# Performance work log

Hardware: AMD Instinct MI355X
Metric: run time of the kernel (lower is better)

## Reference

```python
import jax, jax.numpy as jnp
import numpy as np

NUM_HEADS = 8
NEG_MASK = -1000.0  # original code masks with -1000, not -inf


def setup_inputs() -> dict:
    key = jax.random.key(0)
    ks = jax.random.split(key, 12)
    B, S, D = 4, 2048, 512
    HID, OUT = 512, 512
    dh = D // NUM_HEADS      # 64, per-head input dim
    eh = HID // NUM_HEADS    # 64, per-head hidden dim
    w = 0.02
    return {
        "q": jax.random.normal(ks[0], (B, S, D), dtype=jnp.float32),
        "k": jax.random.normal(ks[1], (B, S, D), dtype=jnp.float32),
        "v": jax.random.normal(ks[2], (B, S, D), dtype=jnp.float32),
        # Linear weights stored as [in, out] (transpose of torch convention)
        "Wq": jax.random.normal(ks[3], (dh, eh), dtype=jnp.float32) * w,
        "bq": jax.random.normal(ks[4], (eh,), dtype=jnp.float32) * w,
        "Wk": jax.random.normal(ks[5], (dh, eh), dtype=jnp.float32) * w,
        "bk": jax.random.normal(ks[6], (eh,), dtype=jnp.float32) * w,
        "Wv": jax.random.normal(ks[7], (dh, eh), dtype=jnp.float32) * w,
        "bv": jax.random.normal(ks[8], (eh,), dtype=jnp.float32) * w,
        "Wo": jax.random.normal(ks[9], (HID, OUT), dtype=jnp.float32) * w,
        "bo": jax.random.normal(ks[10], (OUT,), dtype=jnp.float32) * w,
        "valid_lens": jnp.maximum(jax.random.randint(ks[11], (B,), 0, S), 1),
        "max_len": S,
    }


def reference(q, k, v, Wq, bq, Wk, bk, Wv, bv, Wo, bo, valid_lens, max_len):
    B, S, D = q.shape
    H = NUM_HEADS
    # split into heads: [B, S, H, dh]; note the SAME projection weights are
    # shared across heads (as in the original module)
    qh = q.reshape(B, S, H, D // H)
    kh = k.reshape(B, S, H, D // H)
    vh = v.reshape(B, S, H, D // H)
    qp = jnp.einsum('bshd,de->bshe', qh, Wq) + bq  # [B,S,H,eh]
    kp = jnp.einsum('bshd,de->bshe', kh, Wk) + bk
    vp = jnp.einsum('bshd,de->bshe', vh, Wv) + bv
    scale = 1.0 / jnp.sqrt(jnp.asarray(qp.shape[-1], qp.dtype))
    scores = jnp.einsum('bshe,bthe->bhst', qp, kp) * scale  # [B,H,S,S]
    # key-padding mask: positions j >= valid_len get -1000 (original semantics)
    key_mask = jnp.arange(S)[None, :] < valid_lens[:, None]  # [B,S]
    scores = jnp.where(key_mask[:, None, None, :], scores, NEG_MASK)
    attn = jax.nn.softmax(scores, axis=-1)
    ctx = jnp.einsum('bhst,bthe->bshe', attn, vp).reshape(B, S, -1)  # head-major concat
    return jnp.einsum('bse,eo->bso', ctx, Wo) + bo
```

## Files before the change

kernel.cpp:

```cpp
#include <hip/hip_runtime.h>

#define S_LEN 2048
#define D_MODEL 512

typedef __attribute__((ext_vector_type(8))) short s8v;
typedef __attribute__((ext_vector_type(4))) float f4v;
typedef __attribute__((ext_vector_type(4))) short s4v;
typedef __attribute__((ext_vector_type(4))) int   i4v;
typedef __attribute__((ext_vector_type(2))) int   i2v;

#define MFMA __builtin_amdgcn_mfma_f32_16x16x32_bf16

__device__ inline short f2bf(float x) {
    union { float f; unsigned u; } v; v.f = x;
    unsigned r = v.u + 0x7fffu + ((v.u >> 16) & 1u);
    return (short)(r >> 16);
}
__device__ inline unsigned pack_bf2_trunc(float a, float b) {
    unsigned ua = __builtin_bit_cast(unsigned, a);
    unsigned ub = __builtin_bit_cast(unsigned, b);
    return (ua >> 16) | (ub & 0xffff0000u);
}

template <int C>
__device__ inline float dppf(float x) {
    int i = __builtin_bit_cast(int, x);
    i = __builtin_amdgcn_update_dpp(0, i, C, 0xF, 0xF, true);
    return __builtin_bit_cast(float, i);
}
__device__ inline float rowsum16(float x) {
    x += dppf<0xB1>(x);
    x += dppf<0x4E>(x);
    x += dppf<0x141>(x);
    x += dppf<0x140>(x);
    return x;
}

typedef const __attribute__((address_space(1))) void* gptr_t;
typedef __attribute__((address_space(3))) void* sptr_t;
__device__ inline void gload16(const void* g, void* s) {
    __builtin_amdgcn_global_load_lds((gptr_t)g, (sptr_t)s, 16, 0, 0);
}

__global__ __launch_bounds__(256) void prep_kernel(
    const float* __restrict__ Wo, const float* __restrict__ Wq,
    const float* __restrict__ Wk, const float* __restrict__ Wv,
    short* __restrict__ WoT, short* __restrict__ WqT,
    short* __restrict__ WkT, short* __restrict__ WvT)
{
    if (blockIdx.x < 64) {
        __shared__ short t[64 * 65];
        const int bi = (blockIdx.x >> 3) * 64;
        const int bj = (blockIdx.x & 7) * 64;
        const int c = threadIdx.x & 63, rr = threadIdx.x >> 6;
#pragma unroll
        for (int r = 0; r < 16; r++) {
            int i = r * 4 + rr;
            t[c * 65 + i] = f2bf(Wo[(size_t)(bi + i) * 512 + bj + c]);
        }
        __syncthreads();
#pragma unroll
        for (int r = 0; r < 16; r++) {
            int o = r * 4 + rr;
            WoT[(size_t)(bj + o) * 512 + bi + c] = t[o * 65 + c];
        }
    } else {
        for (int j = threadIdx.x; j < 12288; j += 256) {
            int w = j >> 12, r = j & 4095;
            int e = r >> 6, d = r & 63;
            const float* W = (w == 0) ? Wq : (w == 1) ? Wk : Wv;
            short* WT = (w == 0) ? WqT : (w == 1) ? WkT : WvT;
            WT[r] = f2bf(W[d * 64 + e]);
        }
    }
}

__global__ __launch_bounds__(256) void proj_kernel(
    const float* __restrict__ q, const float* __restrict__ k, const float* __restrict__ v,
    const float* __restrict__ bq, const float* __restrict__ bk, const float* __restrict__ bv,
    const short* __restrict__ WqT, const short* __restrict__ WkT, const short* __restrict__ WvT,
    short* __restrict__ qp, short* __restrict__ kp, short* __restrict__ vpT)
{
    const int t = blockIdx.z >> 2;
    const int b = blockIdx.z & 3;
    const int h = blockIdx.y;
    const int qt = blockIdx.x;
    const int w = threadIdx.x >> 6, lane = threadIdx.x & 63;
    const int l = lane & 15, qd = lane >> 4;

    const float* X    = (t == 0) ? q   : (t == 1) ? k   : v;
    const float* bias = (t == 0) ? bq  : (t == 1) ? bk  : bv;
    const short* WT   = (t == 0) ? WqT : (t == 1) ? WkT : WvT;

    const int s0 = qt * 128 + w * 32;

    s8v a[2][2];
#pragma unroll
    for (int mt = 0; mt < 2; mt++)
#pragma unroll
        for (int kk = 0; kk < 2; kk++) {
            const float* p = X + (size_t)(b * S_LEN + s0 + mt * 16 + l) * 512 + h * 64 + kk * 32 + qd * 8;
            f4v x0 = *(const f4v*)p;
            f4v x1 = *(const f4v*)(p + 4);
            s8v fr;
            fr[0] = f2bf(x0[0]); fr[1] = f2bf(x0[1]); fr[2] = f2bf(x0[2]); fr[3] = f2bf(x0[3]);
            fr[4] = f2bf(x1[0]); fr[5] = f2bf(x1[1]); fr[6] = f2bf(x1[2]); fr[7] = f2bf(x1[3]);
            a[mt][kk] = fr;
        }
    s8v wf[4][2];
#pragma unroll
    for (int nt = 0; nt < 4; nt++) {
        int wrow = (t < 2) ? (4 * l + nt) : (nt * 16 + l);
#pragma unroll
        for (int kk = 0; kk < 2; kk++)
            wf[nt][kk] = *(const s8v*)(WT + wrow * 64 + kk * 32 + qd * 8);
    }

    const f4v fz = {0.f, 0.f, 0.f, 0.f};
    f4v acc[2][4];
#pragma unroll
    for (int mt = 0; mt < 2; mt++)
#pragma unroll
        for (int nt = 0; nt < 4; nt++) acc[mt][nt] = fz;

#pragma unroll
    for (int kk = 0; kk < 2; kk++)
#pragma unroll
        for (int nt = 0; nt < 4; nt++)
#pragma unroll
            for (int mt = 0; mt < 2; mt++)
                acc[mt][nt] = MFMA(a[mt][kk], wf[nt][kk], acc[mt][nt], 0, 0, 0);

    const float SC = 0.125f * 1.442695041f;

    if (t < 2) {
        short* out = (t == 0) ? qp : kp;
        float bbs[4];
#pragma unroll
        for (int nt = 0; nt < 4; nt++) bbs[nt] = bias[4 * l + nt];
#pragma unroll
        for (int mt = 0; mt < 2; mt++)
#pragma unroll
            for (int r = 0; r < 4; r++) {
                int s = s0 + mt * 16 + qd * 4 + r;
                s4v pk;
#pragma unroll
                for (int nt = 0; nt < 4; nt++) {
                    float val = acc[mt][nt][r] + bbs[nt];
                    if (t == 0) val *= SC;
                    pk[nt] = f2bf(val);
                }
                *(s4v*)(out + ((size_t)(b * 8 + h) * S_LEN + s) * 64 + 4 * l) = pk;
            }
    } else {
#pragma unroll
        for (int nt = 0; nt < 4; nt++) {
            float bb = bias[nt * 16 + l];
            int e = nt * 16 + l;
#pragma unroll
            for (int mt = 0; mt < 2; mt++) {
                s4v pk;
#pragma unroll
                for (int r = 0; r < 4; r++) pk[r] = f2bf(acc[mt][nt][r] + bb);
                *(s4v*)(vpT + ((size_t)(b * 8 + h) * 64 + e) * S_LEN + s0 + mt * 16 + qd * 4) = pk;
            }
        }
    }
}

__global__ __launch_bounds__(128) void repack_kernel(
    const short* __restrict__ kp, const short* __restrict__ vpT,
    short* __restrict__ kfrag, short* __restrict__ vfrag)
{
    const int kb = blockIdx.x, h = blockIdx.y, b = blockIdx.z;
    const int bh = b * 8 + h;
    const int half = threadIdx.x >> 6, f = threadIdx.x & 63;
    const int l = f & 15, qd = f >> 4;
    const size_t slab = (size_t)bh * S_LEN * 64;
    const size_t obase = ((size_t)bh * 32 + kb) * 4096;
    if (half == 0) {
        const short* src = kp + slab;
#pragma unroll
        for (int c = 0; c < 8; c++) {
            int nt = c >> 1, kk = c & 1;
            s8v x = *(const s8v*)(src + (size_t)(kb * 64 + 4 * l + nt) * 64 + kk * 32 + qd * 8);
            *(s8v*)(kfrag + obase + c * 512 + f * 8) = x;
        }
    } else {
        const short* src = vpT + slab;
#pragma unroll
        for (int c = 0; c < 8; c++) {
            int ne = c >> 1, kk = c & 1;
            s8v x = *(const s8v*)(src + (size_t)(4 * l + ne) * S_LEN + kb * 64 + kk * 32 + qd * 8);
            *(s8v*)(vfrag + obase + c * 512 + f * 8) = x;
        }
    }
}

__global__ __launch_bounds__(256, 3) void attn_kernel(
    const short* __restrict__ qp, const short* __restrict__ kfrag,
    const short* __restrict__ vfrag,
    const int* __restrict__ valid_lens, short* __restrict__ ctx)
{
    __shared__ alignas(16) short kbuf[2][4096];
    __shared__ alignas(16) short vbuf[2][4096];
    __shared__ alignas(16) short lP[4][32 * 72];

    const int gid = blockIdx.x;
    const int h  = gid & 7;
    const int b  = (gid >> 3) & 3;
    const int qt = gid >> 5;
    const int w = threadIdx.x >> 6, lane = threadIdx.x & 63;
    const int l = lane & 15, qd = lane >> 4;
    const int vlen = valid_lens[b];
    const int ntiles = (vlen + 63) >> 6;

    const int bh = b * 8 + h;
    const short* Qs = qp + (size_t)bh * S_LEN * 64;
    const short* Kf = kfrag + (size_t)bh * 32 * 4096;
    const short* Vf = vfrag + (size_t)bh * 32 * 4096;

    const int s0 = qt * 128 + w * 32;
    s8v qf[2][2];
#pragma unroll
    for (int mt = 0; mt < 2; mt++)
#pragma unroll
        for (int kk = 0; kk < 2; kk++)
            qf[mt][kk] = *(const s8v*)(Qs + (size_t)(s0 + mt * 16 + l) * 64 + kk * 32 + qd * 8);

    const f4v fz = {0.f, 0.f, 0.f, 0.f};
    f4v O[2][4];
    float lsum[2][4];
#pragma unroll
    for (int mt = 0; mt < 2; mt++)
#pragma unroll
        for (int r = 0; r < 4; r++) lsum[mt][r] = 0.f;
#pragma unroll
    for (int mt = 0; mt < 2; mt++)
#pragma unroll
        for (int ne = 0; ne < 4; ne++) O[mt][ne] = fz;

    short* lPw = lP[w];
    const int toff = threadIdx.x * 8;

    gload16(Kf + toff,        &kbuf[0][toff]);
    gload16(Kf + 2048 + toff, &kbuf[0][2048 + toff]);
    gload16(Vf + toff,        &vbuf[0][toff]);
    gload16(Vf + 2048 + toff, &vbuf[0][2048 + toff]);
    __syncthreads();

    for (int kb = 0; kb < ntiles; kb++) {
        const int cur = kb & 1;
        if (kb + 1 < ntiles) {
            const short* Ks = Kf + (size_t)(kb + 1) * 4096;
            const short* Vs = Vf + (size_t)(kb + 1) * 4096;
            gload16(Ks + toff,        &kbuf[cur ^ 1][toff]);
            gload16(Ks + 2048 + toff, &kbuf[cur ^ 1][2048 + toff]);
            gload16(Vs + toff,        &vbuf[cur ^ 1][toff]);
            gload16(Vs + 2048 + toff, &vbuf[cur ^ 1][2048 + toff]);
        }

        const short* Kb = &kbuf[cur][lane * 8];
        s8v kf[4][2];
#pragma unroll
        for (int nt = 0; nt < 4; nt++)
#pragma unroll
            for (int kk = 0; kk < 2; kk++)
                kf[nt][kk] = *(const s8v*)(Kb + (nt * 2 + kk) * 512);

        f4v sf[2][4];
#pragma unroll
        for (int mt = 0; mt < 2; mt++)
#pragma unroll
            for (int nt = 0; nt < 4; nt++) sf[mt][nt] = fz;
#pragma unroll
        for (int nt = 0; nt < 4; nt++)
#pragma unroll
            for (int mt = 0; mt < 2; mt++) {
                sf[mt][nt] = MFMA(qf[mt][0], kf[nt][0], sf[mt][nt], 0, 0, 0);
                sf[mt][nt] = MFMA(qf[mt][1], kf[nt][1], sf[mt][nt], 0, 0, 0);
            }

        const short* Vb = &vbuf[cur][lane * 8];
        s8v vf[4][2];
#pragma unroll
        for (int ne = 0; ne < 4; ne++)
#pragma unroll
            for (int kk = 0; kk < 2; kk++)
                vf[ne][kk] = *(const s8v*)(Vb + (ne * 2 + kk) * 512);

        if (kb == ntiles - 1 && (vlen & 63)) {
            int rem = vlen - kb * 64;
#pragma unroll
            for (int nt = 0; nt < 4; nt++)
                if (4 * l + nt >= rem) {
#pragma unroll
                    for (int mt = 0; mt < 2; mt++)
#pragma unroll
                        for (int r = 0; r < 4; r++) sf[mt][nt][r] = -1e30f;
                }
        }

#pragma unroll
        for (int mt = 0; mt < 2; mt++)
#pragma unroll
            for (int r = 0; r < 4; r++) {
                float p0 = __builtin_amdgcn_exp2f(sf[mt][0][r]);
                float p1 = __builtin_amdgcn_exp2f(sf[mt][1][r]);
                float p2 = __builtin_amdgcn_exp2f(sf[mt][2][r]);
                float p3 = __builtin_amdgcn_exp2f(sf[mt][3][r]);
                lsum[mt][r] += (p0 + p1) + (p2 + p3);
                i2v pk;
                pk[0] = (int)pack_bf2_trunc(p0, p1);
                pk[1] = (int)pack_bf2_trunc(p2, p3);
                *(i2v*)(lPw + (mt * 16 + qd * 4 + r) * 72 + 4 * l) = pk;
            }

        s8v pa[2][2];
#pragma unroll
        for (int mt = 0; mt < 2; mt++)
#pragma unroll
            for (int kk = 0; kk < 2; kk++)
                pa[mt][kk] = *(const s8v*)(lPw + (mt * 16 + l) * 72 + kk * 32 + qd * 8);
#pragma unroll
        for (int ne = 0; ne < 4; ne++)
#pragma unroll
            for (int mt = 0; mt < 2; mt++) {
                O[mt][ne] = MFMA(pa[mt][0], vf[ne][0], O[mt][ne], 0, 0, 0);
                O[mt][ne] = MFMA(pa[mt][1], vf[ne][1], O[mt][ne], 0, 0, 0);
            }

        __syncthreads();
    }

#pragma unroll
    for (int mt = 0; mt < 2; mt++)
#pragma unroll
        for (int r = 0; r < 4; r++) {
            float inv = 1.0f / rowsum16(lsum[mt][r]);
            int s = s0 + mt * 16 + qd * 4 + r;
            s4v pk;
#pragma unroll
            for (int ne = 0; ne < 4; ne++) pk[ne] = f2bf(O[mt][ne][r] * inv);
            *(s4v*)(ctx + ((size_t)(b * S_LEN + s)) * 512 + h * 64 + 4 * l) = pk;
        }
}

__global__ __launch_bounds__(256) void outproj_kernel(
    const short* __restrict__ ctx, const short* __restrict__ WoT,
    const float* __restrict__ bo, float* __restrict__ out)
{
    __shared__ short lB[64 * 520];
    __shared__ short lA[128 * 40];

    const int rb = blockIdx.x * 128;
    const int nb = blockIdx.y * 64;
    const int w = threadIdx.x >> 6, lane = threadIdx.x & 63;
    const int l = lane & 15, qd = lane >> 4;

    {
        int n = threadIdx.x >> 2, c0 = threadIdx.x & 3;
#pragma unroll
        for (int i = 0; i < 16; i++) {
            int g = i * 4 + c0;
            i4v x = *(const i4v*)(WoT + (size_t)(nb + n) * 512 + g * 8);
            *(i4v*)(lB + n * 520 + g * 8) = x;
        }
    }
    __syncthreads();

    const f4v fz = {0.f, 0.f, 0.f, 0.f};
    f4v acc[2][4];
#pragma unroll
    for (int mt = 0; mt < 2; mt++)
#pragma unroll
        for (int nt = 0; nt < 4; nt++) acc[mt][nt] = fz;

    for (int ko = 0; ko < 16; ko++) {
        {
            int r = threadIdx.x >> 1, hp = threadIdx.x & 1;
            const short* src = ctx + (size_t)(rb + r) * 512 + ko * 32 + hp * 16;
            i4v x0 = *(const i4v*)src;
            i4v x1 = *(const i4v*)(src + 8);
            *(i4v*)(lA + r * 40 + hp * 16) = x0;
            *(i4v*)(lA + r * 40 + hp * 16 + 8) = x1;
        }
        __syncthreads();
        s8v af[2];
#pragma unroll
        for (int mt = 0; mt < 2; mt++)
            af[mt] = *(const s8v*)(lA + (w * 32 + mt * 16 + l) * 40 + qd * 8);
#pragma unroll
        for (int nt = 0; nt < 4; nt++) {
            s8v bfr = *(const s8v*)(lB + (nt * 16 + l) * 520 + ko * 32 + qd * 8);
#pragma unroll
            for (int mt = 0; mt < 2; mt++)
                acc[mt][nt] = MFMA(af[mt], bfr, acc[mt][nt], 0, 0, 0);
        }
        __syncthreads();
    }

#pragma unroll
    for (int nt = 0; nt < 4; nt++) {
        float bias = bo[nb + nt * 16 + l];
#pragma unroll
        for (int mt = 0; mt < 2; mt++)
#pragma unroll
            for (int r = 0; r < 4; r++) {
                int row = rb + w * 32 + mt * 16 + qd * 4 + r;
                out[(size_t)row * 512 + nb + nt * 16 + l] = acc[mt][nt][r] + bias;
            }
    }
}

extern "C" void kernel_launch(void* const* d_in, const int* in_sizes, int n_in,
                              void* d_out, int out_size, void* d_ws, size_t ws_size,
                              hipStream_t stream)
{
    const float* q  = (const float*)d_in[0];
    const float* k  = (const float*)d_in[1];
    const float* v  = (const float*)d_in[2];
    const float* Wq = (const float*)d_in[3];
    const float* bq = (const float*)d_in[4];
    const float* Wk = (const float*)d_in[5];
    const float* bk = (const float*)d_in[6];
    const float* Wv = (const float*)d_in[7];
    const float* bv = (const float*)d_in[8];
    const float* Wo = (const float*)d_in[9];
    const float* bo = (const float*)d_in[10];
    const int*   vl = (const int*)d_in[11];
    float* out = (float*)d_out;

    char* ws = (char*)d_ws;
    const size_t SL = (size_t)4 * 8 * S_LEN * 64 * sizeof(short);
    short* qp    = (short*)(ws);
    short* kp    = (short*)(ws + SL);
    short* ctx   = (short*)(ws + SL);
    short* vpT   = (short*)(ws + 2 * SL);
    short* kfrag = (short*)(ws + 3 * SL);
    short* vfrag = (short*)(ws + 4 * SL);
    short* WoT = (short*)(ws + 5 * SL);
    short* WqT = WoT + 512 * 512;
    short* WkT = WqT + 4096;
    short* WvT = WkT + 4096;

    prep_kernel<<<65, 256, 0, stream>>>(Wo, Wq, Wk, Wv, WoT, WqT, WkT, WvT);
    proj_kernel<<<dim3(16, 8, 12), 256, 0, stream>>>(q, k, v, bq, bk, bv,
                                                     WqT, WkT, WvT, qp, kp, vpT);
    repack_kernel<<<dim3(32, 8, 4), 128, 0, stream>>>(kp, vpT, kfrag, vfrag);
    attn_kernel<<<512, 256, 0, stream>>>(qp, kfrag, vfrag, vl, ctx);
    outproj_kernel<<<dim3(64, 8), 256, 0, stream>>>(ctx, WoT, bo, out);
}
```

Baseline: 185.9 us.

## Use two waves per attention block with 64 query rows each

The attention kernel now runs 128 threads per block, and each wave handles 64 query rows instead of 32. This halves the number of LDS K/V fragment reads per query row and the block-level syncs per tile. Score computation is split into two 32-row groups to limit register pressure, and MFMA sections are wrapped in s_setprio. Batch indices are also XOR-swizzled across the second half of the grid to balance the uneven valid lengths. The cost is more registers per wave and fewer waves per block for hiding latency.

```diff
diff --git a/kernel.cpp b/kernel.cpp
--- a/kernel.cpp
+++ b/kernel.cpp
@@ -197,19 +197,20 @@
     }
 }
 
-__global__ __launch_bounds__(256, 3) void attn_kernel(
+__global__ __launch_bounds__(128, 2) void attn_kernel(
     const short* __restrict__ qp, const short* __restrict__ kfrag,
     const short* __restrict__ vfrag,
     const int* __restrict__ valid_lens, short* __restrict__ ctx)
 {
     __shared__ alignas(16) short kbuf[2][4096];
     __shared__ alignas(16) short vbuf[2][4096];
-    __shared__ alignas(16) short lP[4][32 * 72];
+    __shared__ alignas(16) short lP[2][64 * 72];
 
     const int gid = blockIdx.x;
     const int h  = gid & 7;
-    const int b  = (gid >> 3) & 3;
+    int b        = (gid >> 3) & 3;
     const int qt = gid >> 5;
+    b ^= 3 * ((gid >> 8) & 1);
     const int w = threadIdx.x >> 6, lane = threadIdx.x & 63;
     const int l = lane & 15, qd = lane >> 4;
     const int vlen = valid_lens[b];
@@ -220,33 +221,33 @@
     const short* Kf = kfrag + (size_t)bh * 32 * 4096;
     const short* Vf = vfrag + (size_t)bh * 32 * 4096;
 
-    const int s0 = qt * 128 + w * 32;
-    s8v qf[2][2];
-#pragma unroll
-    for (int mt = 0; mt < 2; mt++)
+    const int s0 = qt * 128 + w * 64;
+    s8v qf[4][2];
+#pragma unroll
+    for (int mt = 0; mt < 4; mt++)
 #pragma unroll
         for (int kk = 0; kk < 2; kk++)
             qf[mt][kk] = *(const s8v*)(Qs + (size_t)(s0 + mt * 16 + l) * 64 + kk * 32 + qd * 8);
 
     const f4v fz = {0.f, 0.f, 0.f, 0.f};
-    f4v O[2][4];
-    float lsum[2][4];
-#pragma unroll
-    for (int mt = 0; mt < 2; mt++)
+    f4v O[4][4];
+    float lsum[4][4];
+#pragma unroll
+    for (int mt = 0; mt < 4; mt++)
 #pragma unroll
         for (int r = 0; r < 4; r++) lsum[mt][r] = 0.f;
 #pragma unroll
-    for (int mt = 0; mt < 2; mt++)
+    for (int mt = 0; mt < 4; mt++)
 #pragma unroll
         for (int ne = 0; ne < 4; ne++) O[mt][ne] = fz;
 
     short* lPw = lP[w];
     const int toff = threadIdx.x * 8;
 
-    gload16(Kf + toff,        &kbuf[0][toff]);
-    gload16(Kf + 2048 + toff, &kbuf[0][2048 + toff]);
-    gload16(Vf + toff,        &vbuf[0][toff]);
-    gload16(Vf + 2048 + toff, &vbuf[0][2048 + toff]);
+#pragma unroll
+    for (int r = 0; r < 4; r++) gload16(Kf + r * 1024 + toff, &kbuf[0][r * 1024 + toff]);
+#pragma unroll
+    for (int r = 0; r < 4; r++) gload16(Vf + r * 1024 + toff, &vbuf[0][r * 1024 + toff]);
     __syncthreads();
 
     for (int kb = 0; kb < ntiles; kb++) {
@@ -254,10 +255,10 @@
         if (kb + 1 < ntiles) {
             const short* Ks = Kf + (size_t)(kb + 1) * 4096;
             const short* Vs = Vf + (size_t)(kb + 1) * 4096;
-            gload16(Ks + toff,        &kbuf[cur ^ 1][toff]);
-            gload16(Ks + 2048 + toff, &kbuf[cur ^ 1][2048 + toff]);
-            gload16(Vs + toff,        &vbuf[cur ^ 1][toff]);
-            gload16(Vs + 2048 + toff, &vbuf[cur ^ 1][2048 + toff]);
+#pragma unroll
+            for (int r = 0; r < 4; r++) gload16(Ks + r * 1024 + toff, &kbuf[cur ^ 1][r * 1024 + toff]);
+#pragma unroll
+            for (int r = 0; r < 4; r++) gload16(Vs + r * 1024 + toff, &vbuf[cur ^ 1][r * 1024 + toff]);
         }
 
         const short* Kb = &kbuf[cur][lane * 8];
@@ -268,18 +269,52 @@
             for (int kk = 0; kk < 2; kk++)
                 kf[nt][kk] = *(const s8v*)(Kb + (nt * 2 + kk) * 512);
 
-        f4v sf[2][4];
-#pragma unroll
-        for (int mt = 0; mt < 2; mt++)
-#pragma unroll
-            for (int nt = 0; nt < 4; nt++) sf[mt][nt] = fz;
-#pragma unroll
-        for (int nt = 0; nt < 4; nt++)
-#pragma unroll
-            for (int mt = 0; mt < 2; mt++) {
-                sf[mt][nt] = MFMA(qf[mt][0], kf[nt][0], sf[mt][nt], 0, 0, 0);
-                sf[mt][nt] = MFMA(qf[mt][1], kf[nt][1], sf[mt][nt], 0, 0, 0);
+        const bool mask_on = (kb == ntiles - 1) && (vlen & 63);
+        const int rem = vlen - kb * 64;
+
+#pragma unroll
+        for (int g = 0; g < 2; g++) {
+            f4v sf[2][4];
+#pragma unroll
+            for (int mt = 0; mt < 2; mt++)
+#pragma unroll
+                for (int nt = 0; nt < 4; nt++) sf[mt][nt] = fz;
+            __builtin_amdgcn_s_setprio(1);
+#pragma unroll
+            for (int nt = 0; nt < 4; nt++)
+#pragma unroll
+                for (int mt = 0; mt < 2; mt++) {
+                    sf[mt][nt] = MFMA(qf[g * 2 + mt][0], kf[nt][0], sf[mt][nt], 0, 0, 0);
+                    sf[mt][nt] = MFMA(qf[g * 2 + mt][1], kf[nt][1], sf[mt][nt], 0, 0, 0);
+                }
+            __builtin_amdgcn_s_setprio(0);
+
+            if (mask_on) {
+#pragma unroll
+                for (int nt = 0; nt < 4; nt++)
+                    if (4 * l + nt >= rem) {
+#pragma unroll
+                        for (int mt = 0; mt < 2; mt++)
+#pragma unroll
+                            for (int r = 0; r < 4; r++) sf[mt][nt][r] = -1e30f;
+                    }
             }
+
+#pragma unroll
+            for (int mt = 0; mt < 2; mt++)
+#pragma unroll
+                for (int r = 0; r < 4; r++) {
+                    float p0 = __builtin_amdgcn_exp2f(sf[mt][0][r]);
+                    float p1 = __builtin_amdgcn_exp2f(sf[mt][1][r]);
+                    float p2 = __builtin_amdgcn_exp2f(sf[mt][2][r]);
+                    float p3 = __builtin_amdgcn_exp2f(sf[mt][3][r]);
+                    lsum[g * 2 + mt][r] += (p0 + p1) + (p2 + p3);
+                    i2v pk;
+                    pk[0] = (int)pack_bf2_trunc(p0, p1);
+                    pk[1] = (int)pack_bf2_trunc(p2, p3);
+                    *(i2v*)(lPw + ((g * 2 + mt) * 16 + qd * 4 + r) * 72 + 4 * l) = pk;
+                }
+        }
 
         const short* Vb = &vbuf[cur][lane * 8];
         s8v vf[4][2];
@@ -289,52 +324,27 @@
             for (int kk = 0; kk < 2; kk++)
                 vf[ne][kk] = *(const s8v*)(Vb + (ne * 2 + kk) * 512);
 
-        if (kb == ntiles - 1 && (vlen & 63)) {
-            int rem = vlen - kb * 64;
-#pragma unroll
-            for (int nt = 0; nt < 4; nt++)
-                if (4 * l + nt >= rem) {
-#pragma unroll
-                    for (int mt = 0; mt < 2; mt++)
-#pragma unroll
-                        for (int r = 0; r < 4; r++) sf[mt][nt][r] = -1e30f;
-                }
-        }
-
-#pragma unroll
-        for (int mt = 0; mt < 2; mt++)
-#pragma unroll
-            for (int r = 0; r < 4; r++) {
-                float p0 = __builtin_amdgcn_exp2f(sf[mt][0][r]);
-                float p1 = __builtin_amdgcn_exp2f(sf[mt][1][r]);
-                float p2 = __builtin_amdgcn_exp2f(sf[mt][2][r]);
-                float p3 = __builtin_amdgcn_exp2f(sf[mt][3][r]);
-                lsum[mt][r] += (p0 + p1) + (p2 + p3);
-                i2v pk;
-                pk[0] = (int)pack_bf2_trunc(p0, p1);
-                pk[1] = (int)pack_bf2_trunc(p2, p3);
-                *(i2v*)(lPw + (mt * 16 + qd * 4 + r) * 72 + 4 * l) = pk;
-            }
-
-        s8v pa[2][2];
-#pragma unroll
-        for (int mt = 0; mt < 2; mt++)
+        s8v pa[4][2];
+#pragma unroll
+        for (int mt = 0; mt < 4; mt++)
 #pragma unroll
             for (int kk = 0; kk < 2; kk++)
                 pa[mt][kk] = *(const s8v*)(lPw + (mt * 16 + l) * 72 + kk * 32 + qd * 8);
+        __builtin_amdgcn_s_setprio(1);
 #pragma unroll
         for (int ne = 0; ne < 4; ne++)
 #pragma unroll
-            for (int mt = 0; mt < 2; mt++) {
+            for (int mt = 0; mt < 4; mt++) {
                 O[mt][ne] = MFMA(pa[mt][0], vf[ne][0], O[mt][ne], 0, 0, 0);
                 O[mt][ne] = MFMA(pa[mt][1], vf[ne][1], O[mt][ne], 0, 0, 0);
             }
+        __builtin_amdgcn_s_setprio(0);
 
         __syncthreads();
     }
 
 #pragma unroll
-    for (int mt = 0; mt < 2; mt++)
+    for (int mt = 0; mt < 4; mt++)
 #pragma unroll
         for (int r = 0; r < 4; r++) {
             float inv = 1.0f / rowsum16(lsum[mt][r]);
@@ -448,6 +458,6 @@
     proj_kernel<<<dim3(16, 8, 12), 256, 0, stream>>>(q, k, v, bq, bk, bv,
                                                      WqT, WkT, WvT, qp, kp, vpT);
     repack_kernel<<<dim3(32, 8, 4), 128, 0, stream>>>(kp, vpT, kfrag, vfrag);
-    attn_kernel<<<512, 256, 0, stream>>>(qp, kfrag, vfrag, vl, ctx);
+    attn_kernel<<<512, 128, 0, stream>>>(qp, kfrag, vfrag, vl, ctx);
     outproj_kernel<<<dim3(64, 8), 256, 0, stream>>>(ctx, WoT, bo, out);
 }
```

Measured after the change: 198.0 us. 6.5% more time.
